# Kernel optimization log

Hardware: AMD Instinct MI355X
Metric: run time of the kernel (lower is better)

The kernel has to match this reference:

```python
import jax, jax.numpy as jnp
import numpy as np

RESO = 32
SPLIT = 4
HEADS = 16  # block-level heads; each branch uses HEADS//2
DIM = 512
MLP_HID = 2048
EPS = 1e-5


def layer_norm(x, g, b):
    m = jnp.mean(x, axis=-1, keepdims=True)
    v = jnp.mean(jnp.square(x - m), axis=-1, keepdims=True)
    return (x - m) * jax.lax.rsqrt(v + EPS) * g + b


def dwconv3x3(x, w, b):
    # x: [N, C, Hs, Ws], w: [C, 1, 3, 3] (torch depthwise layout), b: [C]
    y = jax.lax.conv_general_dilated(
        x, w, window_strides=(1, 1), padding='SAME',
        feature_group_count=x.shape[1],
        dimension_numbers=('NCHW', 'OIHW', 'NCHW'))
    return y + b[None, :, None, None]


def cswin_branch(q, k, v, reso, Hs, Ws, heads, lepe_w, lepe_b):
    # q,k,v: [B, L, C] with L = reso^3; attention windows are Hs*Ws tokens,
    # window batch = B * D * (H/Hs) * (W/Ws) (depth folded into batch).
    B, L, C = q.shape
    hd = C // heads
    D = H = W = reso
    scale = hd ** -0.5

    def to_win(t):  # [B,L,C] -> [Bw, heads, Hs*Ws, hd]
        t = t.transpose(0, 2, 1).reshape(B, C, D, H // Hs, Hs, W // Ws, Ws)
        t = t.transpose(0, 2, 3, 5, 4, 6, 1).reshape(-1, Hs * Ws, heads, hd)
        return t.transpose(0, 2, 1, 3)

    qh = to_win(q)
    kh = to_win(k)
    # v windows kept in [Bw, C, Hs, Ws] image layout for the LePE depthwise conv
    vw = v.transpose(0, 2, 1).reshape(B, C, D, H // Hs, Hs, W // Ws, Ws)
    vw = vw.transpose(0, 2, 3, 5, 1, 4, 6).reshape(-1, C, Hs, Ws)
    lepe = dwconv3x3(vw, lepe_w, lepe_b)
    lepe = lepe.reshape(-1, heads, hd, Hs * Ws).transpose(0, 1, 3, 2)
    vh = vw.reshape(-1, heads, hd, Hs * Ws).transpose(0, 1, 3, 2)

    attn = jax.nn.softmax((qh * scale) @ jnp.swapaxes(kh, -1, -2), axis=-1)
    o = attn @ vh + lepe  # [Bw, heads, Hs*Ws, hd]

    # windows2img back to [B, L, C]
    o = o.transpose(0, 2, 1, 3).reshape(-1, Hs * Ws, C)
    o = o.reshape(B, D, H // Hs, W // Ws, Hs, Ws, C)
    o = o.transpose(0, 1, 2, 4, 3, 5, 6).reshape(B, D * H * W, C)
    return o


def setup_inputs() -> dict:
    key = jax.random.key(0)
    ks = jax.random.split(key, 16)
    C, Cb, hid = DIM, DIM // 2, MLP_HID

    def lin(k, fan_in, shape):
        return (jax.random.normal(k, shape, jnp.float32) * (fan_in ** -0.5))

    return {
        'x': jax.random.normal(ks[0], (1, C, RESO, RESO, RESO), jnp.float32),
        'norm1_g': jnp.ones((C,), jnp.float32),
        'norm1_b': jnp.zeros((C,), jnp.float32),
        'qkv_w': lin(ks[1], C, (C, 3 * C)),
        'lepe0_w': lin(ks[2], 9, (Cb, 1, 3, 3)),
        'lepe0_b': jnp.zeros((Cb,), jnp.float32),
        'lepe1_w': lin(ks[3], 9, (Cb, 1, 3, 3)),
        'lepe1_b': jnp.zeros((Cb,), jnp.float32),
        'proj_w': lin(ks[4], C, (C, C)),
        'proj_b': jnp.zeros((C,), jnp.float32),
        'norm2_g': jnp.ones((C,), jnp.float32),
        'norm2_b': jnp.zeros((C,), jnp.float32),
        'fc1_w': lin(ks[5], C, (C, hid)),
        'fc1_b': jnp.zeros((hid,), jnp.float32),
        'fc2_w': lin(ks[6], hid, (hid, C)),
        'fc2_b': jnp.zeros((C,), jnp.float32),
    }


def reference(x, norm1_g, norm1_b, qkv_w, lepe0_w, lepe0_b, lepe1_w, lepe1_b,
              proj_w, proj_b, norm2_g, norm2_b, fc1_w, fc1_b, fc2_w, fc2_b):
    B, C = x.shape[0], x.shape[1]
    reso = x.shape[2]
    xc = jnp.transpose(x, (0, 2, 3, 4, 1))  # [B,D,H,W,C]
    img = layer_norm(xc, norm1_g, norm1_b)
    qkv = jnp.einsum('bdhwc,co->bdhwo', img, qkv_w).reshape(B, -1, 3, C)
    q, k, v = qkv[:, :, 0], qkv[:, :, 1], qkv[:, :, 2]

    Ch = C // 2
    hh = HEADS // 2
    # branch 0: idx=0 -> H_sp=reso, W_sp=split ; branch 1: idx=1 -> H_sp=split, W_sp=reso
    x1 = cswin_branch(q[..., :Ch], k[..., :Ch], v[..., :Ch], reso, reso, SPLIT, hh, lepe0_w, lepe0_b)
    x2 = cswin_branch(q[..., Ch:], k[..., Ch:], v[..., Ch:], reso, SPLIT, reso, hh, lepe1_w, lepe1_b)
    att = jnp.concatenate([x1, x2], axis=2) @ proj_w + proj_b

    xf = xc.reshape(B, -1, C) + att
    h = layer_norm(xf, norm2_g, norm2_b)
    h = jax.nn.gelu(h @ fc1_w + fc1_b, approximate=False) @ fc2_w + fc2_b
    xf = xf + h
    out = xf.reshape(B, reso, reso, reso, C).transpose(0, 4, 1, 2, 3)
    return out
```

## Files before the change

### kernel.cpp

```cpp
#include <hip/hip_runtime.h>
#include <hip/hip_bf16.h>
#include <stdint.h>

typedef uint16_t u16;
typedef __attribute__((ext_vector_type(8))) short short8;
typedef __attribute__((ext_vector_type(4))) float floatx4;

#define MFMA(a, b, c) __builtin_amdgcn_mfma_f32_16x16x32_bf16((a), (b), (c), 0, 0, 0)
#define AS1(p) ((const __attribute__((address_space(1))) void*)(p))
#define AS3(p) ((__attribute__((address_space(3))) void*)(p))

static __device__ __forceinline__ float u2f(u16 u) {
    return __uint_as_float(((uint32_t)u) << 16);
}
static __device__ __forceinline__ u16 f2u(float f) {
    union { __hip_bfloat16 h; u16 u; } cv;
    cv.h = __float2bfloat16(f);
    return cv.u;
}
static __device__ __forceinline__ float ldf(const void* p, size_t i, bool f32m) {
    return f32m ? ((const float*)p)[i] : u2f(((const u16*)p)[i]);
}
static __device__ __forceinline__ short8 ld8(const void* p, size_t i, bool f32m) {
    if (f32m) {
        const float* f = (const float*)p + i;
        short8 o;
#pragma unroll
        for (int j = 0; j < 8; ++j) o[j] = (short)f2u(f[j]);
        return o;
    }
    return *reinterpret_cast<const short8*>((const u16*)p + i);
}
static __device__ __forceinline__ void st8(void* p, size_t i, const float* v, bool f32m) {
    if (f32m) {
        float* f = (float*)p + i;
#pragma unroll
        for (int j = 0; j < 8; ++j) f[j] = v[j];
    } else {
        short8 o;
#pragma unroll
        for (int j = 0; j < 8; ++j) o[j] = (short)f2u(v[j]);
        *reinterpret_cast<short8*>((u16*)p + i) = o;
    }
}
static __device__ __forceinline__ float gelu_f(float u) {
    float y = 1.5957691216057308f * (u + 0.044715f * u * u * u);
    return u / (1.f + __expf(-y));
}
static __device__ __forceinline__ void pl32swap(uint32_t& a, uint32_t& b) {
    asm volatile("v_permlane32_swap_b32 %0, %1" : "+v"(a), "+v"(b));
}

__global__ __launch_bounds__(256) void detect_dtype(const u16* __restrict__ x,
                                                    int* __restrict__ flag)
{
    const int tid = threadIdx.x;
    int cnt = 0;
    for (int i = tid; i < 4096; i += 256) {
        int e = (x[i] >> 7) & 0xFF;
        if (e >= 0xBE) ++cnt;
    }
#pragma unroll
    for (int m = 32; m >= 1; m >>= 1) cnt += __shfl_xor(cnt, m);
    __shared__ int s[4];
    if ((tid & 63) == 0) s[tid >> 6] = cnt;
    __syncthreads();
    if (tid == 0) flag[0] = (s[0] + s[1] + s[2] + s[3] >= 64) ? 1 : 0;
}

template <int MODE>
__global__ __launch_bounds__(256) void transpose_k(
    const void* __restrict__ src, void* __restrict__ dst, long dstOff,
    int R, int Cc, int dstS,
    const u16* __restrict__ add,
    const int* __restrict__ dflag, int srcSel, int dstSel)
{
    const bool iF = dflag[0] != 0;
    const bool sF = srcSel && iF;
    const bool dF = dstSel && iF;
    __shared__ __align__(16) u16 tile[64][72];
    const int tid = threadIdx.x;
    const int r0 = blockIdx.y * 64;
    const int c0 = blockIdx.x * 64;
#pragma unroll
    for (int s = 0; s < 2; ++s) {
        int ch = tid + s * 256;
        int ir = ch >> 3, ic = (ch & 7) * 8;
        short8 v = ld8(src, (size_t)(r0 + ir) * Cc + c0 + ic, sF);
        if constexpr (MODE == 3) {
            short8 a = *reinterpret_cast<const short8*>(add + (size_t)(r0 + ir) * Cc + c0 + ic);
#pragma unroll
            for (int j = 0; j < 8; ++j)
                tile[ir][ic + j] = f2u(u2f((u16)v[j]) + u2f((u16)a[j]));
        } else {
#pragma unroll
            for (int j = 0; j < 8; ++j) tile[ir][ic + j] = (u16)v[j];
        }
    }
    __syncthreads();
#pragma unroll
    for (int s = 0; s < 2; ++s) {
        int ch = tid + s * 256;
        int jr = ch >> 3, jc = (ch & 7) * 8;
        float f[8];
        if constexpr (MODE == 2) {
#pragma unroll
            for (int j = 0; j < 8; ++j)
                f[j] = u2f(tile[jc + j][jr]) + u2f(add[(size_t)(c0 + jr) * 512 + r0 + jc + j]);
        } else {
#pragma unroll
            for (int j = 0; j < 8; ++j) f[j] = u2f(tile[jc + j][jr]);
        }
        st8(dst, (size_t)dstOff + (size_t)(c0 + jr) * dstS + r0 + jc, f, dF);
    }
}

__global__ __launch_bounds__(256) void ln512(
    const u16* __restrict__ X, const void* __restrict__ g, const void* __restrict__ b,
    u16* __restrict__ O, const int* __restrict__ dflag)
{
    const bool iF = dflag[0] != 0;
    const int wid = threadIdx.x >> 6, lane = threadIdx.x & 63;
    const int row = blockIdx.x * 4 + wid;
    const size_t base = (size_t)row * 512 + lane * 8;
    short8 v = *reinterpret_cast<const short8*>(X + base);
    float f[8];
    float s = 0.f, sq = 0.f;
#pragma unroll
    for (int j = 0; j < 8; ++j) { f[j] = u2f((u16)v[j]); s += f[j]; sq += f[j] * f[j]; }
#pragma unroll
    for (int m = 32; m >= 1; m >>= 1) { s += __shfl_xor(s, m); sq += __shfl_xor(sq, m); }
    const float mean = s * (1.f / 512.f);
    const float var = sq * (1.f / 512.f) - mean * mean;
    const float rstd = rsqrtf(var + 1e-5f);
    short8 o;
#pragma unroll
    for (int j = 0; j < 8; ++j)
        o[j] = (short)f2u((f[j] - mean) * rstd * ldf(g, lane * 8 + j, iF)
                          + ldf(b, lane * 8 + j, iF));
    *reinterpret_cast<short8*>(O + base) = o;
}

template <int EPI>
__global__ __launch_bounds__(256) void gemm_bt(
    const u16* __restrict__ A, const u16* __restrict__ Bt,
    const void* __restrict__ bias,
    u16* __restrict__ Cout, int Nt, int N, int K, const int* __restrict__ dflag)
{
    const bool iF = dflag[0] != 0;
    __shared__ __align__(16) u16 As[2][128 * 32];
    __shared__ __align__(16) u16 Bs[2][128 * 32];
    const int bidf = blockIdx.x;
    const int xcd = bidf & 7;
    const int j = bidf >> 3;
    const int m_blk = (j / Nt) * 8 + xcd;
    const int n_blk = j % Nt;
    const int tid = threadIdx.x;
    const int lane = tid & 63, wid = tid >> 6;
    const int wm = wid >> 1, wn = wid & 1;
    const int quad = lane >> 4, l15 = lane & 15;

    floatx4 zero4 = {0.f, 0.f, 0.f, 0.f};
    floatx4 acc[4][4];
#pragma unroll
    for (int i = 0; i < 4; ++i)
#pragma unroll
        for (int jj = 0; jj < 4; ++jj) acc[i][jj] = zero4;

    const u16* Ab = A + (size_t)m_blk * 128 * K;
    const u16* Bb = Bt + (size_t)n_blk * 128 * K;
    const int r0 = tid >> 2;
    const int k0o = (tid & 3) * 8;

    for (int kk = 0; kk < K; kk += 64) {
        if (kk) __syncthreads();
#pragma unroll
        for (int h = 0; h < 2; ++h) {
            const int kg = kk + h * 32 + k0o;
            char* dA = (char*)As[h] + wid * 1024;
            char* dB = (char*)Bs[h] + wid * 1024;
            __builtin_amdgcn_global_load_lds(AS1(Ab + (size_t)r0 * K + kg),        AS3(dA), 16, 0, 0);
            __builtin_amdgcn_global_load_lds(AS1(Ab + (size_t)(r0 + 64) * K + kg), AS3(dA + 4096), 16, 0, 0);
            __builtin_amdgcn_global_load_lds(AS1(Bb + (size_t)r0 * K + kg),        AS3(dB), 16, 0, 0);
            __builtin_amdgcn_global_load_lds(AS1(Bb + (size_t)(r0 + 64) * K + kg), AS3(dB + 4096), 16, 0, 0);
        }
        __syncthreads();
#pragma unroll
        for (int h = 0; h < 2; ++h) {
            short8 af[4], bfv[4];
#pragma unroll
            for (int i = 0; i < 4; ++i)
                af[i] = *reinterpret_cast<const short8*>(&As[h][(wm * 64 + i * 16 + l15) * 32 + quad * 8]);
#pragma unroll
            for (int jj = 0; jj < 4; ++jj)
                bfv[jj] = *reinterpret_cast<const short8*>(&Bs[h][(wn * 64 + jj * 16 + l15) * 32 + quad * 8]);
#pragma unroll
            for (int i = 0; i < 4; ++i)
#pragma unroll
                for (int jj = 0; jj < 4; ++jj)
                    acc[i][jj] = MFMA(af[i], bfv[jj], acc[i][jj]);
        }
    }

    const int m_base = m_blk * 128 + wm * 64 + quad * 4;
    const int n_base = n_blk * 128 + wn * 64 + l15;
#pragma unroll
    for (int i = 0; i < 4; ++i) {
#pragma unroll
        for (int jj = 0; jj < 4; ++jj) {
            const int n = n_base + jj * 16;
            float badd = 0.f;
            if constexpr (EPI >= 1) badd = ldf(bias, n, iF);
#pragma unroll
            for (int r = 0; r < 4; ++r) {
                const int m = m_base + i * 16 + r;
                float v = acc[i][jj][r] + badd;
                if constexpr (EPI == 3) v = gelu_f(v);
                Cout[(size_t)m * N + n] = f2u(v);
            }
        }
    }
}

#define STG(slot, mat, kh, Gb, kcol) do {                                        \
    char* _d = (char*)&L[(slot)][(mat)][(kh)][0] + ldsofs;                       \
    __builtin_amdgcn_global_load_lds(AS1((Gb) + (size_t)srow0 * K + (kcol) + scol0),         AS3(_d),        16, 0, 0); \
    __builtin_amdgcn_global_load_lds(AS1((Gb) + (size_t)(srow0 + 128) * K + (kcol) + scol0), AS3(_d + 8192), 16, 0, 0); \
} while (0)

#define VMW(n) do { asm volatile("s_waitcnt vmcnt(" #n ")" ::: "memory");        \
                    __builtin_amdgcn_sched_barrier(0); } while (0)

#define PHASE(s, kh, nq, STAGE_STMT, WAIT_STMT) do {                             \
    const char* Au = (const char*)&L[(s)][0][(kh)][0];                           \
    const char* Bu = (const char*)&L[(s)][1][(kh)][0];                           \
    if ((nq) == 0) {                                                             \
        _Pragma("unroll")                                                        \
        for (int mf = 0; mf < 8; ++mf)                                           \
            af[mf] = *reinterpret_cast<const short8*>(Au + aoff[mf]);            \
    }                                                                            \
    short8 b0 = *reinterpret_cast<const short8*>(Bu + boff[nq][0]);              \
    short8 b1 = *reinterpret_cast<const short8*>(Bu + boff[nq][1]);              \
    STAGE_STMT;                                                                  \
    asm volatile("s_barrier" ::: "memory");                                      \
    asm volatile("s_waitcnt lgkmcnt(0)" ::: "memory");                           \
    __builtin_amdgcn_sched_barrier(0);                                           \
    __builtin_amdgcn_s_setprio(1);                                               \
    _Pragma("unroll")                                                            \
    for (int mf = 0; mf < 8; ++mf) {                                             \
        acc[mf][(nq) * 2]     = MFMA(af[mf], b0, acc[mf][(nq) * 2]);             \
        acc[mf][(nq) * 2 + 1] = MFMA(af[mf], b1, acc[mf][(nq) * 2 + 1]);         \
    }                                                                            \
    __builtin_amdgcn_s_setprio(0);                                               \
    WAIT_STMT;                                                                   \
    asm volatile("s_barrier" ::: "memory");                                      \
} while (0)

#define GROUP(g, W2, W4, S12, S34) do {                                          \
    const int _s = (g) & 1;                                                      \
    PHASE(_s, 0, 0, if (S12) STG(_s ^ 1, 0, 1, Ab, ((g) + 1) * 64 + 32), (void)0); \
    PHASE(_s, 0, 1, if (S12) STG(_s ^ 1, 1, 1, Bb, ((g) + 1) * 64 + 32), W2);    \
    PHASE(_s, 1, 0, if (S34) STG(_s,     0, 0, Ab, ((g) + 2) * 64),      (void)0); \
    PHASE(_s, 1, 1, if (S34) STG(_s,     1, 0, Bb, ((g) + 2) * 64),      W4);    \
} while (0)

template <int EPI>
__global__ __launch_bounds__(512, 2) void gemm256_bt(
    const u16* __restrict__ A, const u16* __restrict__ Bt,
    const void* __restrict__ bias,
    u16* __restrict__ Cout, int Nt, int N, int K, const int* __restrict__ dflag)
{
    const bool iF = dflag[0] != 0;
    __shared__ __align__(16) u16 L[2][2][2][8192];
    const int bidf = blockIdx.x;
    const int xcd = bidf & 7;
    const int j = bidf >> 3;
    const int m_blk = (j / Nt) * 8 + xcd;
    const int n_blk = j % Nt;
    const int tid = threadIdx.x;
    const int lane = tid & 63, wid = tid >> 6;
    const int wm = wid >> 2, wn = wid & 3;
    const int quad = lane >> 4, l15 = lane & 15;

    const int srow0 = wid * 16 + (lane >> 2);
    const int scol0 = ((lane & 3) ^ ((srow0 >> 1) & 3)) * 8;
    const int ldsofs = wid * 1024;

    const u16* Ab = A + (size_t)m_blk * 256 * K;
    const u16* Bb = Bt + (size_t)n_blk * 256 * K;

    const int sq = (quad ^ ((l15 >> 1) & 3)) << 4;
    int aoff[8], boff[2][2];
#pragma unroll
    for (int mf = 0; mf < 8; ++mf)
        aoff[mf] = (wm * 128 + mf * 16 + l15) * 64 + sq;
#pragma unroll
    for (int nq = 0; nq < 2; ++nq)
#pragma unroll
        for (int jj = 0; jj < 2; ++jj)
            boff[nq][jj] = (wn * 64 + nq * 32 + jj * 16 + l15) * 64 + sq;

    floatx4 zero4 = {0.f, 0.f, 0.f, 0.f};
    floatx4 acc[8][4];
#pragma unroll
    for (int i = 0; i < 8; ++i)
#pragma unroll
        for (int jj = 0; jj < 4; ++jj) acc[i][jj] = zero4;
    short8 af[8];

    const int NG = K >> 6;

    STG(0, 0, 0, Ab, 0);
    STG(0, 1, 0, Bb, 0);
    STG(0, 0, 1, Ab, 32);
    STG(0, 1, 1, Bb, 32);
    STG(1, 0, 0, Ab, 64);
    STG(1, 1, 0, Bb, 64);
    VMW(8);
    asm volatile("s_barrier" ::: "memory");

    int g = 0;
    for (; g < NG - 2; ++g) GROUP(g, VMW(8), VMW(8), true, true);
    GROUP(g, VMW(8), VMW(4), true, false); ++g;
    GROUP(g, VMW(0), (void)0, false, false);

    const int m0 = m_blk * 256 + wm * 128 + quad * 4;
    const int n0 = n_blk * 256 + wn * 64 + l15;
#pragma unroll
    for (int mf = 0; mf < 8; ++mf) {
#pragma unroll
        for (int nf = 0; nf < 4; ++nf) {
            const int n = n0 + nf * 16;
            float badd = 0.f;
            if constexpr (EPI >= 1) badd = ldf(bias, n, iF);
#pragma unroll
            for (int r = 0; r < 4; ++r) {
                const int m = m0 + mf * 16 + r;
                float v = acc[mf][nf][r] + badd;
                if constexpr (EPI == 3) v = gelu_f(v);
                Cout[(size_t)m * N + n] = f2u(v);
            }
        }
    }
}

__global__ __launch_bounds__(256) void cswin_attn(
    const u16* __restrict__ qkv,
    const void* __restrict__ lepe0_w, const void* __restrict__ lepe0_b,
    const void* __restrict__ lepe1_w, const void* __restrict__ lepe1_b,
    u16* __restrict__ att, const int* __restrict__ dflag)
{
    const bool iF = dflag[0] != 0;
    __shared__ __align__(16) u16 q_s[4096];
    __shared__ __align__(16) u16 k_s[4096];
    __shared__ __align__(16) u16 vt_s[32 * 130];
    __shared__ float lw_s[32 * 9];
    __shared__ float lb_s[32];

    const int bid = blockIdx.x;
    const int branch = bid >> 11;
    const int rr = bid & 2047;
    const int win = rr >> 3, head = rr & 7;
    const int d = win >> 3, blk = win & 7;
    const int tid = threadIdx.x;
    const int lane = tid & 63, wid = tid >> 6;
    const int quad = lane >> 4, l15 = lane & 15;
    const int choff = branch * 256 + head * 32;
    const int dbase = d * 1024;

    const void* lw = branch ? lepe1_w : lepe0_w;
    const void* lbp = branch ? lepe1_b : lepe0_b;
    for (int i = tid; i < 288; i += 256) lw_s[i] = ldf(lw, head * 288 + i, iF);
    if (tid < 32) lb_s[tid] = ldf(lbp, head * 32 + tid, iF);

#pragma unroll
    for (int s = 0; s < 2; ++s) {
        int ch = tid + s * 256;
        int t = ch >> 2, e0 = (ch & 3) * 8;
        int l = branch ? (dbase + blk * 128 + t)
                       : (dbase + (t >> 2) * 32 + blk * 4 + (t & 3));
        size_t rowo = (size_t)l * 1536 + choff + e0;
        short8 qv = *reinterpret_cast<const short8*>(qkv + rowo);
        short8 kv = *reinterpret_cast<const short8*>(qkv + rowo + 512);
        short8 vv = *reinterpret_cast<const short8*>(qkv + rowo + 1024);
        const int sw = ((ch >> 3) & 3) << 3;
        *reinterpret_cast<short8*>(&q_s[(ch * 8) ^ sw]) = qv;
        *reinterpret_cast<short8*>(&k_s[(ch * 8) ^ sw]) = kv;
#pragma unroll
        for (int j = 0; j < 8; ++j) vt_s[(e0 + j) * 130 + t] = (u16)vv[j];
    }
    __syncthreads();

    floatx4 zero4 = {0.f, 0.f, 0.f, 0.f};
    const int sq8 = (quad ^ ((l15 >> 1) & 3)) * 8;
    short8 qf[2];
#pragma unroll
    for (int qi = 0; qi < 2; ++qi)
        qf[qi] = *reinterpret_cast<const short8*>(&q_s[(wid * 32 + qi * 16 + l15) * 32 + sq8]);
    floatx4 st[8][2];
#pragma unroll
    for (int kt = 0; kt < 8; ++kt) { st[kt][0] = zero4; st[kt][1] = zero4; }
#pragma unroll
    for (int kt = 0; kt < 8; ++kt) {
        short8 kf = *reinterpret_cast<const short8*>(&k_s[(kt * 16 + l15) * 32 + sq8]);
        st[kt][0] = MFMA(kf, qf[0], st[kt][0]);
        st[kt][1] = MFMA(kf, qf[1], st[kt][1]);
    }

    const float scale = 0.17677669529663687f;
    float inv[2];
#pragma unroll
    for (int qi = 0; qi < 2; ++qi) {
        float sum = 0.f;
#pragma unroll
        for (int kt = 0; kt < 8; ++kt)
#pragma unroll
            for (int r = 0; r < 4; ++r) {
                float v = __expf(st[kt][qi][r] * scale);
                st[kt][qi][r] = v;
                sum += v;
            }
        sum += __shfl_xor(sum, 16);
        sum += __shfl_xor(sum, 32);
        inv[qi] = 1.f / sum;
    }
    uint32_t pk[2][8][2];
#pragma unroll
    for (int qi = 0; qi < 2; ++qi)
#pragma unroll
        for (int kt = 0; kt < 8; ++kt)
#pragma unroll
            for (int u = 0; u < 2; ++u)
                pk[qi][kt][u] = (uint32_t)f2u(st[kt][qi][2 * u] * inv[qi])
                              | ((uint32_t)f2u(st[kt][qi][2 * u + 1] * inv[qi]) << 16);
#pragma unroll
    for (int qi = 0; qi < 2; ++qi)
#pragma unroll
        for (int t = 0; t < 4; ++t)
#pragma unroll
            for (int u = 0; u < 2; ++u)
                pl32swap(pk[qi][2 * t][u], pk[qi][2 * t + 1][u]);

    const uint32_t* v32 = (const uint32_t*)vt_s;
    const int hi4 = (lane >> 4) & 1;
    floatx4 oacc[2][2];
#pragma unroll
    for (int qi = 0; qi < 2; ++qi) { oacc[qi][0] = zero4; oacc[qi][1] = zero4; }
#pragma unroll
    for (int ks = 0; ks < 4; ++ks) {
        const int kq = ks * 16 + quad * 4;
        union { uint32_t w[4]; short8 s; } bv[2];
#pragma unroll
        for (int j = 0; j < 2; ++j) {
            const int chan = j * 16 + l15;
#pragma unroll
            for (int q = 0; q < 4; ++q) bv[j].w[q] = v32[chan * 65 + kq + q];
        }
#pragma unroll
        for (int qi = 0; qi < 2; ++qi) {
            const uint32_t a0 = pk[qi][2 * ks][0],     a1 = pk[qi][2 * ks][1];
            const uint32_t b0 = pk[qi][2 * ks + 1][0], b1 = pk[qi][2 * ks + 1][1];
            const uint32_t s0 = (uint32_t)__shfl_xor((int)a0, 16);
            const uint32_t s1 = (uint32_t)__shfl_xor((int)a1, 16);
            const uint32_t t0 = (uint32_t)__shfl_xor((int)b0, 16);
            const uint32_t t1 = (uint32_t)__shfl_xor((int)b1, 16);
            union { uint32_t w[4]; short8 s; } gw;
            gw.w[0] = hi4 ? t0 : a0;
            gw.w[1] = hi4 ? t1 : a1;
            gw.w[2] = hi4 ? b0 : s0;
            gw.w[3] = hi4 ? b1 : s1;
            oacc[qi][0] = MFMA(gw.s, bv[0].s, oacc[qi][0]);
            oacc[qi][1] = MFMA(gw.s, bv[1].s, oacc[qi][1]);
        }
    }

    const int Hs = branch ? 4 : 32;
    const int Wsz = branch ? 32 : 4;
    const int wsl = branch ? 5 : 2;
    const int wmask = Wsz - 1;
#pragma unroll
    for (int ii = 0; ii < 2; ++ii) {
        const int t0 = wid * 32 + ii * 16 + quad * 4;
        const int hi0 = t0 >> wsl;
        const int w0 = t0 & wmask;
        const int y0 = (hi0 > 0) ? -1 : 0;
        const int y1 = (hi0 < Hs - 1) ? 1 : 0;
        const bool xm = (w0 > 0);
        const bool xp = (w0 + 4 < Wsz);
#pragma unroll
        for (int j = 0; j < 2; ++j) {
            const int e = j * 16 + l15;
            float val[4];
#pragma unroll
            for (int r = 0; r < 4; ++r) val[r] = oacc[ii][j][r] + lb_s[e];
            const uint32_t* vrow = v32 + e * 65;
            const float* wrow = &lw_s[e * 9];
            for (int dy = y0; dy <= y1; ++dy) {
                const int rowb = (hi0 + dy) << wsl;
                const int wlo = rowb >> 1;
                const int whi = wlo + (Wsz >> 1) - 1;
                const int wb = wlo + (w0 >> 1);
                int c0 = wb - 1; if (c0 < wlo) c0 = wlo;
                int c3 = wb + 2; if (c3 > whi) c3 = whi;
                const uint32_t u0 = vrow[c0];
                const uint32_t u1 = vrow[wb];
                const uint32_t u2 = vrow[wb + 1];
                const uint32_t u3 = vrow[c3];
                const float em1 = __uint_as_float(u0 & 0xffff0000u);
                const float f0 = __uint_as_float(u1 << 16);
                const float f1 = __uint_as_float(u1 & 0xffff0000u);
                const float f2 = __uint_as_float(u2 << 16);
                const float f3 = __uint_as_float(u2 & 0xffff0000u);
                const float f4 = __uint_as_float(u3 << 16);
                const float* w3 = wrow + (dy + 1) * 3;
                const float wl = w3[0], wc = w3[1], wp = w3[2];
                const float wl0 = xm ? wl : 0.f;
                const float wp3 = xp ? wp : 0.f;
                val[0] += wl0 * em1 + wc * f0 + wp * f1;
                val[1] += wl * f0 + wc * f1 + wp * f2;
                val[2] += wl * f1 + wc * f2 + wp * f3;
                val[3] += wl * f2 + wc * f3 + wp3 * f4;
            }
#pragma unroll
            for (int r = 0; r < 4; ++r) {
                const int t = t0 + r;
                const int l = branch ? (dbase + blk * 128 + t)
                                     : (dbase + (t >> 2) * 32 + blk * 4 + (t & 3));
                att[(size_t)l * 512 + choff + e] = f2u(val[r]);
            }
        }
    }
}

extern "C" void kernel_launch(void* const* d_in, const int* in_sizes, int n_in,
                              void* d_out, int out_size, void* d_ws, size_t ws_size,
                              hipStream_t stream)
{
    const void* x      = d_in[0];
    const void* n1g    = d_in[1];
    const void* n1b    = d_in[2];
    const void* qkv_w  = d_in[3];
    const void* l0w    = d_in[4];
    const void* l0b    = d_in[5];
    const void* l1w    = d_in[6];
    const void* l1b    = d_in[7];
    const void* proj_w = d_in[8];
    const void* proj_b = d_in[9];
    const void* n2g    = d_in[10];
    const void* n2b    = d_in[11];
    const void* fc1_w  = d_in[12];
    const void* fc1_b  = d_in[13];
    const void* fc2_w  = d_in[14];
    const void* fc2_b  = d_in[15];

    const size_t MB = 1ull << 20;
    if (ws_size < 104 * MB) return;

    char* w = (char*)d_ws;
    u16* qkvT  = (u16*)(w + 0 * MB);
    u16* projT = (u16*)(w + 2 * MB);
    u16* fc1T  = (u16*)(w + 3 * MB);
    u16* fc2T  = (u16*)(w + 5 * MB);
    int* flag  = (int*)(w + 7 * MB);
    u16* qkvb  = (u16*)(w + 8 * MB);
    u16* xfp   = (u16*)(w + 8 * MB);
    u16* xT    = (u16*)(w + 40 * MB);
    u16* xf    = (u16*)(w + 40 * MB);
    u16* ln2oc = (u16*)(w + 8 * MB);
    u16* yf    = (u16*)(w + 72 * MB);
    u16* img   = (u16*)d_out;
    u16* attb  = (u16*)d_out;
    u16* h1c   = (u16*)d_out;

    const dim3 B(256);
    const dim3 B512(512);
    const u16* NUL = nullptr;
    const void* NULV = nullptr;

    detect_dtype<<<dim3(1), B, 0, stream>>>((const u16*)x, flag);

    transpose_k<0><<<dim3(24, 8), B, 0, stream>>>(qkv_w, qkvT, 0, 512, 1536, 512, NUL, flag, 1, 0);
    transpose_k<0><<<dim3(8, 8),  B, 0, stream>>>(proj_w, projT, 0, 512, 512, 512, NUL, flag, 1, 0);
    transpose_k<0><<<dim3(32, 8), B, 0, stream>>>(fc1_w, fc1T, 0, 512, 2048, 512, NUL, flag, 1, 0);
    transpose_k<0><<<dim3(8, 32), B, 0, stream>>>(fc2_w, fc2T, 0, 2048, 512, 2048, NUL, flag, 1, 0);

    transpose_k<0><<<dim3(512, 8), B, 0, stream>>>(x, xT, 0, 512, 32768, 512, NUL, flag, 1, 0);
    ln512<<<dim3(8192), B, 0, stream>>>(xT, n1g, n1b, img, flag);

    gemm256_bt<0><<<dim3(128 * 6), B512, 0, stream>>>(img, qkvT, NULV, qkvb, 6, 1536, 512, flag);

    cswin_attn<<<dim3(4096), B, 0, stream>>>(qkvb, l0w, l0b, l1w, l1b, attb, flag);

    gemm256_bt<1><<<dim3(128 * 2), B512, 0, stream>>>(attb, projT, proj_b, xfp, 2, 512, 512, flag);

    transpose_k<2><<<dim3(512, 8), B, 0, stream>>>(x, xf, 0, 512, 32768, 512, xfp, flag, 1, 0);

    for (int i = 0; i < 2; ++i) {
        const size_t off = (size_t)i * 16384 * 512;
        ln512<<<dim3(4096), B, 0, stream>>>(xf + off, n2g, n2b, ln2oc, flag);
        gemm256_bt<3><<<dim3(64 * 8), B512, 0, stream>>>(ln2oc, fc1T, fc1_b, h1c, 8, 2048, 512, flag);
        gemm_bt<1><<<dim3(128 * 4), B, 0, stream>>>(h1c, fc2T, fc2_b, yf + off, 4, 512, 2048, flag);
    }
    transpose_k<3><<<dim3(8, 512), B, 0, stream>>>(yf, d_out, 0, 32768, 512, 32768, xf, flag, 0, 1);
}
```

Baseline: 658.5 us.

## Fuse input transpose into LayerNorm1 and loop GEMM blocks over multiple N tiles

Adds a tln1 kernel that reads the channel-major input directly, transposes it through shared memory and applies LayerNorm, which removes the separate transpose pass and the xT intermediate buffer. The 256x256 GEMM now processes several N tiles per block (3 for QKV, 2 for fc1). Each block keeps its A rows and prefetches the next B tile's prologue before the current tile's epilogue. This cuts the grid to 256 blocks, which lowers launch/tail overhead and lets A be reused, but the fewer blocks may leave CUs underfilled. The tln1 strided per-element loads may also coalesce poorly.

After: 712.5 us. 1.08x slower.

```diff
diff --git a/kernel.cpp b/kernel.cpp
--- a/kernel.cpp
+++ b/kernel.cpp
@@ -112,6 +112,54 @@
             for (int j = 0; j < 8; ++j) f[j] = u2f(tile[jc + j][jr]);
         }
         st8(dst, (size_t)dstOff + (size_t)(c0 + jr) * dstS + r0 + jc, f, dF);
+    }
+}
+
+__global__ __launch_bounds__(256) void tln1(
+    const void* __restrict__ x, const void* __restrict__ g, const void* __restrict__ b,
+    u16* __restrict__ O, const int* __restrict__ dflag)
+{
+    const bool iF = dflag[0] != 0;
+    __shared__ __align__(16) u16 tile[16][520];
+    const int tid = threadIdx.x;
+    const int lane = tid & 63, w = tid >> 6;
+    const int t0 = blockIdx.x * 16;
+    const int ti = lane & 15;
+    const int c4 = lane >> 4;
+#pragma unroll
+    for (int p = 0; p < 8; ++p) {
+        const int cb = p * 64 + w * 16 + c4;
+#pragma unroll
+        for (int k = 0; k < 4; ++k) {
+            const int c = cb + k * 4;
+            tile[ti][c] = f2u(ldf(x, (size_t)c * 32768 + t0 + ti, iF));
+        }
+    }
+    __syncthreads();
+    float gv[8], bv[8];
+#pragma unroll
+    for (int jj = 0; jj < 8; ++jj) {
+        gv[jj] = ldf(g, lane * 8 + jj, iF);
+        bv[jj] = ldf(b, lane * 8 + jj, iF);
+    }
+#pragma unroll
+    for (int tt = 0; tt < 4; ++tt) {
+        const int t = w * 4 + tt;
+        short8 v = *reinterpret_cast<const short8*>(&tile[t][lane * 8]);
+        float f[8];
+        float s = 0.f, sq = 0.f;
+#pragma unroll
+        for (int jj = 0; jj < 8; ++jj) { f[jj] = u2f((u16)v[jj]); s += f[jj]; sq += f[jj] * f[jj]; }
+#pragma unroll
+        for (int m = 32; m >= 1; m >>= 1) { s += __shfl_xor(s, m); sq += __shfl_xor(sq, m); }
+        const float mean = s * (1.f / 512.f);
+        const float var = sq * (1.f / 512.f) - mean * mean;
+        const float rstd = rsqrtf(var + 1e-5f);
+        short8 o;
+#pragma unroll
+        for (int jj = 0; jj < 8; ++jj)
+            o[jj] = (short)f2u((f[jj] - mean) * rstd * gv[jj] + bv[jj]);
+        *reinterpret_cast<short8*>(O + (size_t)(t0 + t) * 512 + lane * 8) = o;
     }
 }
 
@@ -264,19 +312,27 @@
     PHASE(_s, 1, 1, if (S34) STG(_s,     1, 0, Bb, ((g) + 2) * 64),      W4);    \
 } while (0)
 
+#define PRO6(BX) do {                                                            \
+    STG(0, 0, 0, Ab, 0);  STG(0, 1, 0, BX, 0);                                   \
+    STG(0, 0, 1, Ab, 32); STG(0, 1, 1, BX, 32);                                  \
+    STG(1, 0, 0, Ab, 64); STG(1, 1, 0, BX, 64);                                  \
+} while (0)
+
 template <int EPI>
 __global__ __launch_bounds__(512, 2) void gemm256_bt(
     const u16* __restrict__ A, const u16* __restrict__ Bt,
     const void* __restrict__ bias,
-    u16* __restrict__ Cout, int Nt, int N, int K, const int* __restrict__ dflag)
+    u16* __restrict__ Cout, int Nt, int N, int K, int tpb,
+    const int* __restrict__ dflag)
 {
     const bool iF = dflag[0] != 0;
     __shared__ __align__(16) u16 L[2][2][2][8192];
     const int bidf = blockIdx.x;
     const int xcd = bidf & 7;
     const int j = bidf >> 3;
-    const int m_blk = (j / Nt) * 8 + xcd;
-    const int n_blk = j % Nt;
+    const int Nsup = Nt / tpb;
+    const int m_blk = (j / Nsup) * 8 + xcd;
+    const int n0b = (j % Nsup) * tpb;
     const int tid = threadIdx.x;
     const int lane = tid & 63, wid = tid >> 6;
     const int wm = wid >> 2, wn = wid & 3;
@@ -287,7 +343,6 @@
     const int ldsofs = wid * 1024;
 
     const u16* Ab = A + (size_t)m_blk * 256 * K;
-    const u16* Bb = Bt + (size_t)n_blk * 256 * K;
 
     const int sq = (quad ^ ((l15 >> 1) & 3)) << 4;
     int aoff[8], boff[2][2];
@@ -302,43 +357,48 @@
 
     floatx4 zero4 = {0.f, 0.f, 0.f, 0.f};
     floatx4 acc[8][4];
-#pragma unroll
-    for (int i = 0; i < 8; ++i)
-#pragma unroll
-        for (int jj = 0; jj < 4; ++jj) acc[i][jj] = zero4;
     short8 af[8];
 
     const int NG = K >> 6;
 
-    STG(0, 0, 0, Ab, 0);
-    STG(0, 1, 0, Bb, 0);
-    STG(0, 0, 1, Ab, 32);
-    STG(0, 1, 1, Bb, 32);
-    STG(1, 0, 0, Ab, 64);
-    STG(1, 1, 0, Bb, 64);
-    VMW(8);
-    asm volatile("s_barrier" ::: "memory");
-
-    int g = 0;
-    for (; g < NG - 2; ++g) GROUP(g, VMW(8), VMW(8), true, true);
-    GROUP(g, VMW(8), VMW(4), true, false); ++g;
-    GROUP(g, VMW(0), (void)0, false, false);
-
-    const int m0 = m_blk * 256 + wm * 128 + quad * 4;
-    const int n0 = n_blk * 256 + wn * 64 + l15;
-#pragma unroll
-    for (int mf = 0; mf < 8; ++mf) {
-#pragma unroll
-        for (int nf = 0; nf < 4; ++nf) {
-            const int n = n0 + nf * 16;
-            float badd = 0.f;
-            if constexpr (EPI >= 1) badd = ldf(bias, n, iF);
-#pragma unroll
-            for (int r = 0; r < 4; ++r) {
-                const int m = m0 + mf * 16 + r;
-                float v = acc[mf][nf][r] + badd;
-                if constexpr (EPI == 3) v = gelu_f(v);
-                Cout[(size_t)m * N + n] = f2u(v);
+    for (int nt = 0; nt < tpb; ++nt) {
+        const int n_blk = n0b + nt;
+        const u16* Bb = Bt + (size_t)n_blk * 256 * K;
+        if (nt == 0) PRO6(Bb);
+        VMW(8);
+        asm volatile("s_barrier" ::: "memory");
+
+#pragma unroll
+        for (int i = 0; i < 8; ++i)
+#pragma unroll
+            for (int jj = 0; jj < 4; ++jj) acc[i][jj] = zero4;
+
+        int g = 0;
+        for (; g < NG - 2; ++g) GROUP(g, VMW(8), VMW(8), true, true);
+        GROUP(g, VMW(8), VMW(4), true, false); ++g;
+        GROUP(g, VMW(0), (void)0, false, false);
+
+        if (nt + 1 < tpb) {
+            const u16* Bn = Bb + (size_t)256 * K;
+            PRO6(Bn);
+        }
+
+        const int m0 = m_blk * 256 + wm * 128 + quad * 4;
+        const int n0 = n_blk * 256 + wn * 64 + l15;
+#pragma unroll
+        for (int mf = 0; mf < 8; ++mf) {
+#pragma unroll
+            for (int nf = 0; nf < 4; ++nf) {
+                const int n = n0 + nf * 16;
+                float badd = 0.f;
+                if constexpr (EPI >= 1) badd = ldf(bias, n, iF);
+#pragma unroll
+                for (int r = 0; r < 4; ++r) {
+                    const int m = m0 + mf * 16 + r;
+                    float v = acc[mf][nf][r] + badd;
+                    if constexpr (EPI == 3) v = gelu_f(v);
+                    Cout[(size_t)m * N + n] = f2u(v);
+                }
             }
         }
     }
@@ -564,7 +624,6 @@
     int* flag  = (int*)(w + 7 * MB);
     u16* qkvb  = (u16*)(w + 8 * MB);
     u16* xfp   = (u16*)(w + 8 * MB);
-    u16* xT    = (u16*)(w + 40 * MB);
     u16* xf    = (u16*)(w + 40 * MB);
     u16* ln2oc = (u16*)(w + 8 * MB);
     u16* yf    = (u16*)(w + 72 * MB);
@@ -584,21 +643,20 @@
     transpose_k<0><<<dim3(32, 8), B, 0, stream>>>(fc1_w, fc1T, 0, 512, 2048, 512, NUL, flag, 1, 0);
     transpose_k<0><<<dim3(8, 32), B, 0, stream>>>(fc2_w, fc2T, 0, 2048, 512, 2048, NUL, flag, 1, 0);
 
-    transpose_k<0><<<dim3(512, 8), B, 0, stream>>>(x, xT, 0, 512, 32768, 512, NUL, flag, 1, 0);
-    ln512<<<dim3(8192), B, 0, stream>>>(xT, n1g, n1b, img, flag);
-
-    gemm256_bt<0><<<dim3(128 * 6), B512, 0, stream>>>(img, qkvT, NULV, qkvb, 6, 1536, 512, flag);
+    tln1<<<dim3(2048), B, 0, stream>>>(x, n1g, n1b, img, flag);
+
+    gemm256_bt<0><<<dim3(128 * 2), B512, 0, stream>>>(img, qkvT, NULV, qkvb, 6, 1536, 512, 3, flag);
 
     cswin_attn<<<dim3(4096), B, 0, stream>>>(qkvb, l0w, l0b, l1w, l1b, attb, flag);
 
-    gemm256_bt<1><<<dim3(128 * 2), B512, 0, stream>>>(attb, projT, proj_b, xfp, 2, 512, 512, flag);
+    gemm256_bt<1><<<dim3(128 * 2), B512, 0, stream>>>(attb, projT, proj_b, xfp, 2, 512, 512, 1, flag);
 
     transpose_k<2><<<dim3(512, 8), B, 0, stream>>>(x, xf, 0, 512, 32768, 512, xfp, flag, 1, 0);
 
     for (int i = 0; i < 2; ++i) {
         const size_t off = (size_t)i * 16384 * 512;
         ln512<<<dim3(4096), B, 0, stream>>>(xf + off, n2g, n2b, ln2oc, flag);
-        gemm256_bt<3><<<dim3(64 * 8), B512, 0, stream>>>(ln2oc, fc1T, fc1_b, h1c, 8, 2048, 512, flag);
+        gemm256_bt<3><<<dim3(64 * 4), B512, 0, stream>>>(ln2oc, fc1T, fc1_b, h1c, 8, 2048, 512, 2, flag);
         gemm_bt<1><<<dim3(128 * 4), B, 0, stream>>>(h1c, fc2T, fc2_b, yf + off, 4, 512, 2048, flag);
     }
     transpose_k<3><<<dim3(8, 512), B, 0, stream>>>(yf, d_out, 0, 32768, 512, 32768, xf, flag, 0, 1);
```
